# Kernel tuning notes

Measured on AMD Instinct MI355X. Metric: run time of the kernel, lower is better.

Reference implementation:

```python
import jax, jax.numpy as jnp
import numpy as np

N_NODES = 100000
N_EDGES = 6400000
PENALTY_N = 0.1  # init arg `n`


def setup_inputs() -> dict:
    key = jax.random.key(0)
    k1, k2, k3, k4, k5 = jax.random.split(key, 5)
    edge_index = jax.random.randint(k1, (2, N_EDGES), 0, N_NODES, dtype=jnp.int64 if jax.config.read('jax_enable_x64') else jnp.int32)
    edge_weight = jax.random.uniform(k2, (N_EDGES,), dtype=jnp.float32)
    nodes_yield_rate = jax.random.uniform(k3, (N_NODES,), dtype=jnp.float32)
    nodes_traffic = jax.random.uniform(k4, (N_NODES,), dtype=jnp.float32)
    nodes_cost = jax.random.uniform(k5, (N_NODES,), dtype=jnp.float32)
    return {
        'edge_index': edge_index,
        'edge_weight': edge_weight,
        'nodes_yield_rate': nodes_yield_rate,
        'nodes_traffic': nodes_traffic,
        'nodes_cost': nodes_cost,
    }


def reference(edge_index, edge_weight, nodes_yield_rate, nodes_traffic, nodes_cost):
    # Original loop reads src/dst traffic from the ORIGINAL tensor and accumulates
    # updates into a clone; both branches are equivalent to:
    #   src -= |diff| * n * w ; dst += |diff| * n * w
    # i.e. a pure per-edge scatter-add with no edge-order dependency.
    src = edge_index[0]
    dst = edge_index[1]
    diff = nodes_traffic[src] - nodes_traffic[dst]          # [E]
    transfer = jnp.abs(diff) * PENALTY_N * edge_weight      # [E]
    new_traffic = nodes_traffic.at[src].add(-transfer).at[dst].add(transfer)
    total_service_efficiency = jnp.sum(nodes_yield_rate * new_traffic - nodes_cost)
    return new_traffic, total_service_efficiency
```

## Files before the change

kernel.cpp:

```cpp
#include <hip/hip_runtime.h>
#include <hip/hip_fp16.h>

#define PENALTY_N 0.1f
#define CP 33344
#define MAX_BPP 80
#define ABLK 1024

__global__ __launch_bounds__(256, 8) void compute_t_kernel(
    const int* __restrict__ src_idx,
    const int* __restrict__ dst_idx,
    const float* __restrict__ w,
    const float* __restrict__ traffic,
    __half* __restrict__ tbuf,
    float* __restrict__ out_scalar,
    int nE) {
    const int tid = blockIdx.x * blockDim.x + threadIdx.x;
    const int stride = gridDim.x * blockDim.x;
    if (blockIdx.x == 0 && threadIdx.x == 0) *out_scalar = 0.0f;

    const int nvec = nE >> 2;
    const int4* __restrict__ s4p = (const int4*)src_idx;
    const int4* __restrict__ d4p = (const int4*)dst_idx;
    const float4* __restrict__ w4p = (const float4*)w;
    uint2* __restrict__ t2p = (uint2*)tbuf;

    for (int v = tid; v < nvec; v += stride) {
        int4 s = s4p[v];
        int4 d = d4p[v];
        float4 ww = w4p[v];
        float a0 = traffic[s.x], a1 = traffic[s.y];
        float a2 = traffic[s.z], a3 = traffic[s.w];
        float b0 = traffic[d.x], b1 = traffic[d.y];
        float b2 = traffic[d.z], b3 = traffic[d.w];
        float t0 = fabsf(a0 - b0) * (PENALTY_N * ww.x);
        float t1 = fabsf(a1 - b1) * (PENALTY_N * ww.y);
        float t2 = fabsf(a2 - b2) * (PENALTY_N * ww.z);
        float t3 = fabsf(a3 - b3) * (PENALTY_N * ww.w);
        __half2 h01 = __floats2half2_rn(t0, t1);
        __half2 h23 = __floats2half2_rn(t2, t3);
        uint2 pk;
        pk.x = *(unsigned*)&h01;
        pk.y = *(unsigned*)&h23;
        t2p[v] = pk;
    }
    for (int e = (nvec << 2) + tid; e < nE; e += stride) {
        float t = fabsf(traffic[src_idx[e]] - traffic[dst_idx[e]]) *
                  (PENALTY_N * w[e]);
        tbuf[e] = __float2half_rn(t);
    }
}

__global__ __launch_bounds__(ABLK, 4) void part_scatter_kernel(
    const int* __restrict__ src_idx,
    const int* __restrict__ dst_idx,
    const __half* __restrict__ tbuf,
    float* __restrict__ scratch,
    int nE, int nN, int Bpp) {
    __shared__ float hist[CP];

    const int p = blockIdx.x / Bpp;
    const int b = blockIdx.x % Bpp;
    const int lo = p * CP;
    const unsigned csz = (unsigned)min(CP, nN - lo);
    const int tid = threadIdx.x;

    {
        float4* h4 = (float4*)hist;
        for (int i = tid; i < CP / 4; i += ABLK)
            h4[i] = make_float4(0.f, 0.f, 0.f, 0.f);
    }
    __syncthreads();

    const int nvec = nE >> 2;
    const int4* __restrict__ s4p = (const int4*)src_idx;
    const int4* __restrict__ d4p = (const int4*)dst_idx;
    const uint2* __restrict__ t2p = (const uint2*)tbuf;
    const int stride = Bpp * ABLK;

    for (int v = b * ABLK + tid; v < nvec; v += stride) {
        int4 s = s4p[v];
        int4 d = d4p[v];
        uint2 pk = t2p[v];
        __half2 h01 = *(__half2*)&pk.x;
        __half2 h23 = *(__half2*)&pk.y;
        float t0 = __low2float(h01), t1 = __high2float(h01);
        float t2 = __low2float(h23), t3 = __high2float(h23);

        unsigned u;
        u = (unsigned)(s.x - lo); if (u < csz) atomicAdd(&hist[u], -t0);
        u = (unsigned)(d.x - lo); if (u < csz) atomicAdd(&hist[u],  t0);
        u = (unsigned)(s.y - lo); if (u < csz) atomicAdd(&hist[u], -t1);
        u = (unsigned)(d.y - lo); if (u < csz) atomicAdd(&hist[u],  t1);
        u = (unsigned)(s.z - lo); if (u < csz) atomicAdd(&hist[u], -t2);
        u = (unsigned)(d.z - lo); if (u < csz) atomicAdd(&hist[u],  t2);
        u = (unsigned)(s.w - lo); if (u < csz) atomicAdd(&hist[u], -t3);
        u = (unsigned)(d.w - lo); if (u < csz) atomicAdd(&hist[u],  t3);
    }
    for (int e = (nvec << 2) + b * ABLK + tid; e < nE; e += stride) {
        float t = __half2float(tbuf[e]);
        unsigned u;
        u = (unsigned)(src_idx[e] - lo); if (u < csz) atomicAdd(&hist[u], -t);
        u = (unsigned)(dst_idx[e] - lo); if (u < csz) atomicAdd(&hist[u],  t);
    }

    __syncthreads();
    float* dst = scratch + (size_t)blockIdx.x * CP;
    {
        const int n4 = (int)(csz >> 2);
        float4* d4 = (float4*)dst;
        const float4* h4 = (const float4*)hist;
        for (int i = tid; i < n4; i += ABLK) d4[i] = h4[i];
        for (int i = (n4 << 2) + tid; i < (int)csz; i += ABLK) dst[i] = hist[i];
    }
}

__global__ __launch_bounds__(256) void part_reduce_kernel(
    const float* __restrict__ scratch,
    const float* __restrict__ traffic,
    const float* __restrict__ yield_rate,
    const float* __restrict__ cost,
    float* __restrict__ out,
    int nN, int Bpp) {
    const int tid = blockIdx.x * blockDim.x + threadIdx.x;
    const int stride = gridDim.x * blockDim.x;

    float acc = 0.0f;
    for (int i = tid; i < nN; i += stride) {
        int p = i / CP;
        int off = i - p * CP;
        const float* base = scratch + (size_t)p * Bpp * CP + off;

        float s0 = traffic[i], s1 = 0.0f, s2 = 0.0f, s3 = 0.0f;
        int b = 0;
        for (; b + 8 <= Bpp; b += 8) {
            const float* q = base + (size_t)b * CP;
            float a0 = q[0 * (size_t)CP];
            float a1 = q[1 * (size_t)CP];
            float a2 = q[2 * (size_t)CP];
            float a3 = q[3 * (size_t)CP];
            float a4 = q[4 * (size_t)CP];
            float a5 = q[5 * (size_t)CP];
            float a6 = q[6 * (size_t)CP];
            float a7 = q[7 * (size_t)CP];
            s0 += a0 + a4;
            s1 += a1 + a5;
            s2 += a2 + a6;
            s3 += a3 + a7;
        }
        for (; b < Bpp; ++b) s0 += base[(size_t)b * CP];
        float s = (s0 + s1) + (s2 + s3);
        out[i] = s;
        acc = fmaf(yield_rate[i], s, acc) - cost[i];
    }

    #pragma unroll
    for (int off = 32; off > 0; off >>= 1) acc += __shfl_down(acc, off, 64);

    __shared__ float wsum[4];
    const int lane = threadIdx.x & 63;
    const int wid = threadIdx.x >> 6;
    if (lane == 0) wsum[wid] = acc;
    __syncthreads();
    if (threadIdx.x == 0)
        atomicAdd(&out[nN], wsum[0] + wsum[1] + wsum[2] + wsum[3]);
}

__global__ void init_out_kernel(const float* __restrict__ traffic,
                                float* __restrict__ out, int nN) {
    int i = blockIdx.x * blockDim.x + threadIdx.x;
    if (i < nN) out[i] = traffic[i];
    else if (i == nN) out[i] = 0.0f;
}

__global__ __launch_bounds__(256) void edge_scatter_kernel(
    const int* __restrict__ src_idx, const int* __restrict__ dst_idx,
    const float* __restrict__ w, const float* __restrict__ traffic,
    float* __restrict__ out, int nE) {
    const int tid = blockIdx.x * blockDim.x + threadIdx.x;
    const int stride = gridDim.x * blockDim.x;
    for (int e = tid; e < nE; e += stride) {
        int s = src_idx[e];
        int d = dst_idx[e];
        float t = fabsf(traffic[s] - traffic[d]) * (PENALTY_N * w[e]);
        atomicAdd(&out[s], -t);
        atomicAdd(&out[d], t);
    }
}

__global__ __launch_bounds__(256) void reduce_kernel(
    const float* __restrict__ new_traffic, const float* __restrict__ yield_rate,
    const float* __restrict__ cost, float* __restrict__ total, int nN) {
    const int tid = blockIdx.x * blockDim.x + threadIdx.x;
    const int stride = gridDim.x * blockDim.x;
    float acc = 0.0f;
    for (int i = tid; i < nN; i += stride)
        acc = fmaf(yield_rate[i], new_traffic[i], acc) - cost[i];
    #pragma unroll
    for (int off = 32; off > 0; off >>= 1) acc += __shfl_down(acc, off, 64);
    __shared__ float wsum[4];
    const int lane = threadIdx.x & 63;
    const int wid = threadIdx.x >> 6;
    if (lane == 0) wsum[wid] = acc;
    __syncthreads();
    if (threadIdx.x == 0)
        atomicAdd(total, wsum[0] + wsum[1] + wsum[2] + wsum[3]);
}

extern "C" void kernel_launch(void* const* d_in, const int* in_sizes, int n_in,
                              void* d_out, int out_size, void* d_ws, size_t ws_size,
                              hipStream_t stream) {
    const int* edge_index = (const int*)d_in[0];
    const float* edge_weight = (const float*)d_in[1];
    const float* nodes_yield = (const float*)d_in[2];
    const float* nodes_traffic = (const float*)d_in[3];
    const float* nodes_cost = (const float*)d_in[4];
    float* out = (float*)d_out;

    const int nE = in_sizes[1];
    const int nN = in_sizes[2];
    const int* src_idx = edge_index;
    const int* dst_idx = edge_index + nE;

    const int P = (nN + CP - 1) / CP;

    size_t tbytes = (((size_t)nE * sizeof(__half)) + 255) & ~(size_t)255;
    size_t rem = (ws_size > tbytes) ? (ws_size - tbytes) : 0;
    int Bpp = (int)(rem / ((size_t)P * CP * sizeof(float)));
    if (Bpp > MAX_BPP) Bpp = MAX_BPP;

    if (Bpp >= 16 && P <= 8) {
        __half* tbuf = (__half*)d_ws;
        float* scratch = (float*)((char*)d_ws + tbytes);

        compute_t_kernel<<<2048, 256, 0, stream>>>(
            src_idx, dst_idx, edge_weight, nodes_traffic,
            tbuf, out + nN, nE);
        part_scatter_kernel<<<P * Bpp, ABLK, 0, stream>>>(
            src_idx, dst_idx, tbuf, scratch, nE, nN, Bpp);
        int rgrid = (nN + 255) / 256;
        part_reduce_kernel<<<rgrid, 256, 0, stream>>>(
            scratch, nodes_traffic, nodes_yield, nodes_cost, out, nN, Bpp);
    } else {
        int grid = (nN + 1 + 255) / 256;
        init_out_kernel<<<grid, 256, 0, stream>>>(nodes_traffic, out, nN);
        edge_scatter_kernel<<<2048, 256, 0, stream>>>(src_idx, dst_idx,
                                                      edge_weight, nodes_traffic,
                                                      out, nE);
        reduce_kernel<<<256, 256, 0, stream>>>(out, nodes_yield, nodes_cost,
                                               out + nN, nN);
    }
}
```

Baseline: 235.5 us.

## Pack src, dst and fp16 transfer into 8-byte edge records for scatter

The first kernel now writes one 64-bit record per edge holding a 17-bit src index, a 17-bit dst index and the fp16 transfer value. The partitioned scatter kernel reads these records instead of separate src, dst and half arrays. This cuts the bytes it reads per edge from 10 to 8, and each of the three partitions rereads the whole edge stream. Block indices are also interleaved so groups of 8 blocks cycle through the three partitions, and the scatter loop is unrolled 2x to put more loads in flight. The fast path is now restricted to P==3 and node indices below 2^17, and the compute kernel writes more bytes per edge than before.

```diff
diff --git a/kernel.cpp b/kernel.cpp
--- a/kernel.cpp
+++ b/kernel.cpp
@@ -11,7 +11,7 @@
     const int* __restrict__ dst_idx,
     const float* __restrict__ w,
     const float* __restrict__ traffic,
-    __half* __restrict__ tbuf,
+    uint2* __restrict__ rec,
     float* __restrict__ out_scalar,
     int nE) {
     const int tid = blockIdx.x * blockDim.x + threadIdx.x;
@@ -22,7 +22,7 @@
     const int4* __restrict__ s4p = (const int4*)src_idx;
     const int4* __restrict__ d4p = (const int4*)dst_idx;
     const float4* __restrict__ w4p = (const float4*)w;
-    uint2* __restrict__ t2p = (uint2*)tbuf;
+    uint4* __restrict__ r4p = (uint4*)rec;
 
     for (int v = tid; v < nvec; v += stride) {
         int4 s = s4p[v];
@@ -36,30 +36,46 @@
         float t1 = fabsf(a1 - b1) * (PENALTY_N * ww.y);
         float t2 = fabsf(a2 - b2) * (PENALTY_N * ww.z);
         float t3 = fabsf(a3 - b3) * (PENALTY_N * ww.w);
-        __half2 h01 = __floats2half2_rn(t0, t1);
-        __half2 h23 = __floats2half2_rn(t2, t3);
-        uint2 pk;
-        pk.x = *(unsigned*)&h01;
-        pk.y = *(unsigned*)&h23;
-        t2p[v] = pk;
+        unsigned long long h0 = __half_as_ushort(__float2half_rn(t0));
+        unsigned long long h1 = __half_as_ushort(__float2half_rn(t1));
+        unsigned long long h2 = __half_as_ushort(__float2half_rn(t2));
+        unsigned long long h3 = __half_as_ushort(__float2half_rn(t3));
+        unsigned long long r0 = (unsigned long long)(unsigned)s.x |
+                                ((unsigned long long)(unsigned)d.x << 17) | (h0 << 34);
+        unsigned long long r1 = (unsigned long long)(unsigned)s.y |
+                                ((unsigned long long)(unsigned)d.y << 17) | (h1 << 34);
+        unsigned long long r2 = (unsigned long long)(unsigned)s.z |
+                                ((unsigned long long)(unsigned)d.z << 17) | (h2 << 34);
+        unsigned long long r3 = (unsigned long long)(unsigned)s.w |
+                                ((unsigned long long)(unsigned)d.w << 17) | (h3 << 34);
+        uint4 q0, q1;
+        q0.x = (unsigned)r0; q0.y = (unsigned)(r0 >> 32);
+        q0.z = (unsigned)r1; q0.w = (unsigned)(r1 >> 32);
+        q1.x = (unsigned)r2; q1.y = (unsigned)(r2 >> 32);
+        q1.z = (unsigned)r3; q1.w = (unsigned)(r3 >> 32);
+        r4p[2 * v] = q0;
+        r4p[2 * v + 1] = q1;
     }
     for (int e = (nvec << 2) + tid; e < nE; e += stride) {
-        float t = fabsf(traffic[src_idx[e]] - traffic[dst_idx[e]]) *
-                  (PENALTY_N * w[e]);
-        tbuf[e] = __float2half_rn(t);
+        int si = src_idx[e], di = dst_idx[e];
+        float t = fabsf(traffic[si] - traffic[di]) * (PENALTY_N * w[e]);
+        unsigned long long h = __half_as_ushort(__float2half_rn(t));
+        unsigned long long r = (unsigned long long)(unsigned)si |
+                               ((unsigned long long)(unsigned)di << 17) | (h << 34);
+        rec[e] = make_uint2((unsigned)r, (unsigned)(r >> 32));
     }
 }
 
 __global__ __launch_bounds__(ABLK, 4) void part_scatter_kernel(
-    const int* __restrict__ src_idx,
-    const int* __restrict__ dst_idx,
-    const __half* __restrict__ tbuf,
+    const uint2* __restrict__ rec,
     float* __restrict__ scratch,
     int nE, int nN, int Bpp) {
     __shared__ float hist[CP];
 
-    const int p = blockIdx.x / Bpp;
-    const int b = blockIdx.x % Bpp;
+    const int g = blockIdx.x;
+    const int trio = g >> 3;
+    const int p = trio % 3;
+    const int slice = (g & 7) + 8 * (trio / 3);
     const int lo = p * CP;
     const unsigned csz = (unsigned)min(CP, nN - lo);
     const int tid = threadIdx.x;
@@ -72,39 +88,46 @@
     __syncthreads();
 
     const int nvec = nE >> 2;
-    const int4* __restrict__ s4p = (const int4*)src_idx;
-    const int4* __restrict__ d4p = (const int4*)dst_idx;
-    const uint2* __restrict__ t2p = (const uint2*)tbuf;
+    const uint4* __restrict__ r4p = (const uint4*)rec;
     const int stride = Bpp * ABLK;
 
-    for (int v = b * ABLK + tid; v < nvec; v += stride) {
-        int4 s = s4p[v];
-        int4 d = d4p[v];
-        uint2 pk = t2p[v];
-        __half2 h01 = *(__half2*)&pk.x;
-        __half2 h23 = *(__half2*)&pk.y;
-        float t0 = __low2float(h01), t1 = __high2float(h01);
-        float t2 = __low2float(h23), t3 = __high2float(h23);
-
-        unsigned u;
-        u = (unsigned)(s.x - lo); if (u < csz) atomicAdd(&hist[u], -t0);
-        u = (unsigned)(d.x - lo); if (u < csz) atomicAdd(&hist[u],  t0);
-        u = (unsigned)(s.y - lo); if (u < csz) atomicAdd(&hist[u], -t1);
-        u = (unsigned)(d.y - lo); if (u < csz) atomicAdd(&hist[u],  t1);
-        u = (unsigned)(s.z - lo); if (u < csz) atomicAdd(&hist[u], -t2);
-        u = (unsigned)(d.z - lo); if (u < csz) atomicAdd(&hist[u],  t2);
-        u = (unsigned)(s.w - lo); if (u < csz) atomicAdd(&hist[u], -t3);
-        u = (unsigned)(d.w - lo); if (u < csz) atomicAdd(&hist[u],  t3);
-    }
-    for (int e = (nvec << 2) + b * ABLK + tid; e < nE; e += stride) {
-        float t = __half2float(tbuf[e]);
-        unsigned u;
-        u = (unsigned)(src_idx[e] - lo); if (u < csz) atomicAdd(&hist[u], -t);
-        u = (unsigned)(dst_idx[e] - lo); if (u < csz) atomicAdd(&hist[u],  t);
-    }
-
-    __syncthreads();
-    float* dst = scratch + (size_t)blockIdx.x * CP;
+#define PROC_REC(LOW, HIGH)                                                   \
+    {                                                                         \
+        unsigned lw = (LOW), hw = (HIGH);                                     \
+        unsigned srcI = lw & 0x1FFFFu;                                        \
+        unsigned dstI = ((lw >> 17) | (hw << 15)) & 0x1FFFFu;                 \
+        float t = __half2float(__ushort_as_half((unsigned short)(hw >> 2)));  \
+        unsigned u;                                                           \
+        u = srcI - (unsigned)lo; if (u < csz) atomicAdd(&hist[u], -t);        \
+        u = dstI - (unsigned)lo; if (u < csz) atomicAdd(&hist[u],  t);        \
+    }
+
+    int v = slice * ABLK + tid;
+    for (; v + stride < nvec; v += 2 * stride) {
+        uint4 q0 = r4p[2 * v];
+        uint4 q1 = r4p[2 * v + 1];
+        int v2 = v + stride;
+        uint4 q2 = r4p[2 * v2];
+        uint4 q3 = r4p[2 * v2 + 1];
+        PROC_REC(q0.x, q0.y) PROC_REC(q0.z, q0.w)
+        PROC_REC(q1.x, q1.y) PROC_REC(q1.z, q1.w)
+        PROC_REC(q2.x, q2.y) PROC_REC(q2.z, q2.w)
+        PROC_REC(q3.x, q3.y) PROC_REC(q3.z, q3.w)
+    }
+    for (; v < nvec; v += stride) {
+        uint4 q0 = r4p[2 * v];
+        uint4 q1 = r4p[2 * v + 1];
+        PROC_REC(q0.x, q0.y) PROC_REC(q0.z, q0.w)
+        PROC_REC(q1.x, q1.y) PROC_REC(q1.z, q1.w)
+    }
+    for (int e = (nvec << 2) + slice * ABLK + tid; e < nE; e += stride) {
+        uint2 r = rec[e];
+        PROC_REC(r.x, r.y)
+    }
+#undef PROC_REC
+
+    __syncthreads();
+    float* dst = scratch + (size_t)(p * Bpp + slice) * CP;
     {
         const int n4 = (int)(csz >> 2);
         float4* d4 = (float4*)dst;
@@ -223,20 +246,21 @@
 
     const int P = (nN + CP - 1) / CP;
 
-    size_t tbytes = (((size_t)nE * sizeof(__half)) + 255) & ~(size_t)255;
-    size_t rem = (ws_size > tbytes) ? (ws_size - tbytes) : 0;
+    size_t rbytes = (((size_t)nE * sizeof(uint2)) + 255) & ~(size_t)255;
+    size_t rem = (ws_size > rbytes) ? (ws_size - rbytes) : 0;
     int Bpp = (int)(rem / ((size_t)P * CP * sizeof(float)));
     if (Bpp > MAX_BPP) Bpp = MAX_BPP;
-
-    if (Bpp >= 16 && P <= 8) {
-        __half* tbuf = (__half*)d_ws;
-        float* scratch = (float*)((char*)d_ws + tbytes);
+    Bpp &= ~7;
+
+    if (Bpp >= 16 && P == 3 && nN <= 131072) {
+        uint2* rec = (uint2*)d_ws;
+        float* scratch = (float*)((char*)d_ws + rbytes);
 
         compute_t_kernel<<<2048, 256, 0, stream>>>(
             src_idx, dst_idx, edge_weight, nodes_traffic,
-            tbuf, out + nN, nE);
-        part_scatter_kernel<<<P * Bpp, ABLK, 0, stream>>>(
-            src_idx, dst_idx, tbuf, scratch, nE, nN, Bpp);
+            rec, out + nN, nE);
+        part_scatter_kernel<<<3 * Bpp, ABLK, 0, stream>>>(
+            rec, scratch, nE, nN, Bpp);
         int rgrid = (nN + 255) / 256;
         part_reduce_kernel<<<rgrid, 256, 0, stream>>>(
             scratch, nodes_traffic, nodes_yield, nodes_cost, out, nN, Bpp);
```

After: 249.4 us. 1.06x slower.
